# Kernel tuning notes

Measured on AMD Instinct MI355X. Metric: run time of the kernel, lower is better.

Reference implementation:

```python
import jax, jax.numpy as jnp
import numpy as np

C_M, C_Z, C_H = 256, 128, 32
S, N = 128, 384
EPS = 1e-5


def setup_inputs() -> dict:
    key = jax.random.key(0)
    ks = jax.random.split(key, 8)
    sc = 1.0 / np.sqrt(C_M)
    return {
        "msa": jax.random.normal(ks[0], (S, N, C_M), dtype=jnp.float32),
        "ln_g": jnp.ones((C_M,), dtype=jnp.float32),
        "ln_b": jnp.zeros((C_M,), dtype=jnp.float32),
        "Wl": jax.random.uniform(ks[1], (C_M, C_H), jnp.float32, -sc, sc),
        "bl": jax.random.uniform(ks[2], (C_H,), jnp.float32, -sc, sc),
        "Wr": jax.random.uniform(ks[3], (C_M, C_H), jnp.float32, -sc, sc),
        "br": jax.random.uniform(ks[4], (C_H,), jnp.float32, -sc, sc),
        "Wo": jax.random.uniform(ks[5], (C_H * C_H, C_Z), jnp.float32, -1.0 / C_H, 1.0 / C_H),
        "bo": jax.random.uniform(ks[6], (C_Z,), jnp.float32, -1.0 / C_H, 1.0 / C_H),
    }


def _layernorm(x, g, b):
    mu = jnp.mean(x, axis=-1, keepdims=True)
    var = jnp.mean(jnp.square(x - mu), axis=-1, keepdims=True)
    return (x - mu) * jax.lax.rsqrt(var + EPS) * g + b


def reference(msa, ln_g, ln_b, Wl, bl, Wr, br, Wo, bo):
    s = msa.shape[0]
    m = _layernorm(msa, ln_g, ln_b)          # [s, n, c_m]
    left = m @ Wl + bl                        # [s, n, c_h]
    right = m @ Wr + br                       # [s, n, c_h]
    outer = jnp.einsum('sic,sjd->ijcd', left, right) / s  # [n, n, c_h, c_h]
    outer = outer.reshape(outer.shape[0], outer.shape[1], -1)
    return outer @ Wo + bo                    # [n, n, c_z]
```

## Files before the change

kernel.cpp:

```cpp
#include <hip/hip_runtime.h>
#include <hip/hip_bf16.h>

#define CM 256
#define CZ 128
#define CH 32
#define SS 128
#define NN 384

typedef short bf16x8 __attribute__((ext_vector_type(8)));
typedef float f32x4 __attribute__((ext_vector_type(4)));
typedef unsigned short us4 __attribute__((ext_vector_type(4)));
typedef unsigned short us8 __attribute__((ext_vector_type(8)));

__device__ __forceinline__ unsigned short f2bf(float f) {
    __hip_bfloat16 h = __float2bfloat16(f);
    return __builtin_bit_cast(unsigned short, h);
}

__global__ __launch_bounds__(256) void k0_transpose(
    const float* __restrict__ Wo, const float* __restrict__ Wl, const float* __restrict__ Wr,
    unsigned short* __restrict__ WoT, unsigned short* __restrict__ WT) {
    int n = blockIdx.x;
    for (int k = threadIdx.x; k < CH * CH; k += blockDim.x) {
        WoT[n * (CH * CH) + k] = f2bf(Wo[(size_t)k * CZ + n]);
    }
    int k = threadIdx.x;
    if (n < 32) {
        WT[n * CM + k] = f2bf(Wl[(size_t)k * CH + n]);
    } else if (n < 64) {
        WT[32 * CM + (n - 32) * CM + k] = f2bf(Wr[(size_t)k * CH + (n - 32)]);
    }
}

__global__ __launch_bounds__(256, 2) void k1_ln_proj(
    const float* __restrict__ msa, const float* __restrict__ g, const float* __restrict__ bta,
    const unsigned short* __restrict__ WT, const float* __restrict__ bl, const float* __restrict__ br,
    unsigned short* __restrict__ Lt, unsigned short* __restrict__ Rt)
{
    __shared__ unsigned short A_lds[64 * 264];
    __shared__ unsigned short B_lds[64 * 264];

    const int i    = blockIdx.x;
    const int sh   = blockIdx.y;
    const int t    = threadIdx.x;
    const int wv   = t >> 6;
    const int lane = t & 63;
    const int lr   = lane & 15, lg = lane >> 4;

    const float4 gv = ((const float4*)g)[lane];
    const float4 bv = ((const float4*)bta)[lane];
#pragma unroll 4
    for (int r = 0; r < 16; r++) {
        int sl = wv * 16 + r;
        int s  = sh * 64 + sl;
        float4 v = ((const float4*)(msa + ((size_t)s * NN + i) * CM))[lane];
        float sum = v.x + v.y + v.z + v.w;
        float sq  = v.x * v.x + v.y * v.y + v.z * v.z + v.w * v.w;
#pragma unroll
        for (int off = 32; off >= 1; off >>= 1) {
            sum += __shfl_xor(sum, off, 64);
            sq  += __shfl_xor(sq, off, 64);
        }
        float mu = sum * (1.f / CM);
        float rs = rsqrtf(sq * (1.f / CM) - mu * mu + 1e-5f);
        us4 pk;
        pk[0] = f2bf((v.x - mu) * rs * gv.x + bv.x);
        pk[1] = f2bf((v.y - mu) * rs * gv.y + bv.y);
        pk[2] = f2bf((v.z - mu) * rs * gv.z + bv.z);
        pk[3] = f2bf((v.w - mu) * rs * gv.w + bv.w);
        *(us4*)&A_lds[sl * 264 + lane * 4] = pk;
    }
#pragma unroll
    for (int u = 0; u < 8; u++) {
        int id = u * 256 + t;
        *(us8*)&B_lds[(id >> 5) * 264 + (id & 31) * 8] = *(const us8*)&WT[id * 8];
    }
    __syncthreads();

    const int m0 = (wv >> 1) * 32;
    const int n0 = (wv & 1) * 32;
    f32x4 acc[2][2];
#pragma unroll
    for (int a = 0; a < 2; a++)
#pragma unroll
        for (int b = 0; b < 2; b++) acc[a][b] = (f32x4){0.f, 0.f, 0.f, 0.f};

#pragma unroll
    for (int ks = 0; ks < 8; ks++) {
        int ko = ks * 32 + lg * 8;
        bf16x8 a0 = *(const bf16x8*)&A_lds[(m0 + lr) * 264 + ko];
        bf16x8 a1 = *(const bf16x8*)&A_lds[(m0 + 16 + lr) * 264 + ko];
        bf16x8 b0 = *(const bf16x8*)&B_lds[(n0 + lr) * 264 + ko];
        bf16x8 b1 = *(const bf16x8*)&B_lds[(n0 + 16 + lr) * 264 + ko];
        acc[0][0] = __builtin_amdgcn_mfma_f32_16x16x32_bf16(a0, b0, acc[0][0], 0, 0, 0);
        acc[0][1] = __builtin_amdgcn_mfma_f32_16x16x32_bf16(a0, b1, acc[0][1], 0, 0, 0);
        acc[1][0] = __builtin_amdgcn_mfma_f32_16x16x32_bf16(a1, b0, acc[1][0], 0, 0, 0);
        acc[1][1] = __builtin_amdgcn_mfma_f32_16x16x32_bf16(a1, b1, acc[1][1], 0, 0, 0);
    }

    const bool isL = (n0 == 0);
    const float scale = isL ? 0.0078125f : 1.f;
#pragma unroll
    for (int mt = 0; mt < 2; mt++)
#pragma unroll
        for (int nt = 0; nt < 2; nt++) {
            int ch = (n0 + nt * 16 + lr) & 31;
            float bias = isL ? bl[ch] : br[ch];
            us4 pk;
#pragma unroll
            for (int rg = 0; rg < 4; rg++)
                pk[rg] = f2bf((acc[mt][nt][rg] + bias) * scale);
            unsigned short* dst = (isL ? Lt : Rt) + (size_t)(i * CH + ch) * SS
                                  + sh * 64 + m0 + mt * 16 + lg * 4;
            *(us4*)dst = pk;
        }
}

#define TI 8
#define TJ 8
#define P1_B_OFF 69632
#define OH1_OFF  65536
#define WO_OFF   131072
#define K2_LDS   163840

__global__ __launch_bounds__(512, 2) void k2_fused(
    const unsigned short* __restrict__ Lt, const unsigned short* __restrict__ Rt,
    const unsigned short* __restrict__ WoT, const float* __restrict__ bo,
    float* __restrict__ out)
{
    extern __shared__ char smem[];
    unsigned short* A = (unsigned short*)(smem);
    unsigned short* B = (unsigned short*)(smem + P1_B_OFF);

    const int i0 = blockIdx.x * TI;
    const int j0 = blockIdx.y * TJ;
    const int t  = threadIdx.x;
    const int wv = t >> 6, lane = t & 63;
    const int lr = lane & 15, lg = lane >> 4;

    const unsigned short* gA = Lt + (size_t)i0 * CH * SS;
    const unsigned short* gB = Rt + (size_t)j0 * CH * SS;
#pragma unroll
    for (int it = 0; it < 8; it++) {
        int c  = it * 512 + t;
        int rw = c >> 4, kc = c & 15;
        *(us8*)(A + rw * 136 + kc * 8) = *(const us8*)(gA + rw * 128 + kc * 8);
        *(us8*)(B + rw * 136 + kc * 8) = *(const us8*)(gB + rw * 128 + kc * 8);
    }
    __syncthreads();

    const int m0  = (wv >> 2) * 128;
    const int n0w = (wv & 3) * 64;

    f32x4 accE[4][4], accO[4][4];
#pragma unroll
    for (int a = 0; a < 4; a++)
#pragma unroll
        for (int b = 0; b < 4; b++) {
            accE[a][b] = (f32x4){0.f, 0.f, 0.f, 0.f};
            accO[a][b] = (f32x4){0.f, 0.f, 0.f, 0.f};
        }

#pragma unroll
    for (int ks = 0; ks < 4; ks++) {
        int ko = ks * 32 + lg * 8;
        bf16x8 af[8], bfr[4];
#pragma unroll
        for (int mt = 0; mt < 8; mt++) af[mt]  = *(const bf16x8*)(A + (m0 + mt * 16 + lr) * 136 + ko);
#pragma unroll
        for (int nt = 0; nt < 4; nt++) bfr[nt] = *(const bf16x8*)(B + (n0w + nt * 16 + lr) * 136 + ko);
#pragma unroll
        for (int mt = 0; mt < 8; mt++)
#pragma unroll
            for (int nt = 0; nt < 4; nt++) {
                if (mt & 1)
                    accO[mt >> 1][nt] = __builtin_amdgcn_mfma_f32_16x16x32_bf16(bfr[nt], af[mt], accO[mt >> 1][nt], 0, 0, 0);
                else
                    accE[mt >> 1][nt] = __builtin_amdgcn_mfma_f32_16x16x32_bf16(bfr[nt], af[mt], accE[mt >> 1][nt], 0, 0, 0);
            }
    }
    __syncthreads();

    us8 wreg[4];
#pragma unroll
    for (int q = 0; q < 4; q++) {
        int lam = q * 512 + t;
        int z = lam >> 4, cc = lam & 15;
        int cg = cc ^ (z & 15);
        wreg[q] = *(const us8*)&WoT[(size_t)z * 1024 + cg * 8];
    }

    {
        unsigned short* Oh0 = (unsigned short*)smem;
        unsigned short* Oh1 = (unsigned short*)(smem + OH1_OFF);
#pragma unroll
        for (int mh = 0; mh < 4; mh++) {
            int iiw  = (wv >> 2) * 4 + mh;
            int rowH = iiw * 16 + lr;
            int okey = (rowH ^ (rowH >> 4)) & 7;
#pragma unroll
            for (int nt = 0; nt < 4; nt++) {
                int colBase = n0w + nt * 16 + lg * 4;
                int chk = (colBase >> 3) ^ okey;
                int off = rowH * 256 + chk * 8 + (lg & 1) * 4;
                us4 pkE, pkO;
#pragma unroll
                for (int rg = 0; rg < 4; rg++) {
                    pkE[rg] = f2bf(accE[mh][nt][rg]);
                    pkO[rg] = f2bf(accO[mh][nt][rg]);
                }
                *(us4*)&Oh0[off] = pkE;
                *(us4*)&Oh1[off] = pkO;
            }
        }
    }

    const int zsl = wv & 1, ksl = wv >> 1;
    unsigned short* WB = (unsigned short*)(smem + WO_OFF);

    f32x4 acc2[4][4];
#pragma unroll
    for (int a = 0; a < 4; a++)
#pragma unroll
        for (int b = 0; b < 4; b++) acc2[a][b] = (f32x4){0.f, 0.f, 0.f, 0.f};

    for (int c = 0; c < 8; c++) {
        __syncthreads();
#pragma unroll
        for (int q = 0; q < 4; q++) {
            int lam = q * 512 + t;
            *(us8*)&WB[lam * 8] = wreg[q];
        }
        if (c < 7) {
#pragma unroll
            for (int q = 0; q < 4; q++) {
                int lam = q * 512 + t;
                int z = lam >> 4, cc = lam & 15;
                int cg = cc ^ (z & 15);
                wreg[q] = *(const us8*)&WoT[(size_t)z * 1024 + (c + 1) * 128 + cg * 8];
            }
        }
        __syncthreads();

        const int cch = c * 4 + ksl;
        const int hh  = cch >> 4;
        const int cH  = cch & 15;
        const unsigned short* OhX = (const unsigned short*)(smem + (hh ? OH1_OFF : 0));

        bf16x8 af2[4], bf2[4];
#pragma unroll
        for (int ai = 0; ai < 4; ai++) {
            int rowH = (ai * 2 + ((lane >> 3) & 1)) * 16 + cH;
            int okey = (rowH ^ (rowH >> 4)) & 7;
            int chk  = (((lane & 7) * 4 + lg) ^ okey);
            af2[ai] = *(const bf16x8*)&OhX[rowH * 256 + chk * 8];
        }
#pragma unroll
        for (int bi = 0; bi < 4; bi++) {
            int z = zsl * 64 + bi * 16 + lr;
            int chk = (ksl * 4 + lg) ^ (z & 15);
            bf2[bi] = *(const bf16x8*)&WB[z * 128 + chk * 8];
        }
#pragma unroll
        for (int ai = 0; ai < 4; ai++)
#pragma unroll
            for (int bi = 0; bi < 4; bi++)
                acc2[ai][bi] = __builtin_amdgcn_mfma_f32_16x16x32_bf16(af2[ai], bf2[bi], acc2[ai][bi], 0, 0, 0);
    }
    __syncthreads();

    float* RB = (float*)smem;
#pragma unroll
    for (int ai = 0; ai < 4; ai++)
#pragma unroll
        for (int bi = 0; bi < 4; bi++) {
            int z  = zsl * 64 + bi * 16 + lr;
            int pr = ai * 16 + lg * 4;
            *(f32x4*)&RB[ksl * 8704 + z * 68 + pr] = acc2[ai][bi];
        }
    __syncthreads();

    {
        int z = t >> 2, pq = t & 3;
        float bz = bo[z];
#pragma unroll
        for (int u = 0; u < 4; u++) {
            int p0r = pq * 16 + u * 4;
            f32x4 s = (f32x4){0.f, 0.f, 0.f, 0.f};
#pragma unroll
            for (int ks2 = 0; ks2 < 4; ks2++)
                s += *(const f32x4*)&RB[ks2 * 8704 + z * 68 + p0r];
#pragma unroll
            for (int e = 0; e < 4; e++) {
                int p = p0r + e;
                out[((size_t)(i0 + (p >> 3)) * NN + (j0 + (p & 7))) * CZ + z] = s[e] + bz;
            }
        }
    }
}

extern "C" void kernel_launch(void* const* d_in, const int* in_sizes, int n_in,
                              void* d_out, int out_size, void* d_ws, size_t ws_size,
                              hipStream_t stream) {
    const float* msa  = (const float*)d_in[0];
    const float* ln_g = (const float*)d_in[1];
    const float* ln_b = (const float*)d_in[2];
    const float* Wl   = (const float*)d_in[3];
    const float* bl   = (const float*)d_in[4];
    const float* Wr   = (const float*)d_in[5];
    const float* br   = (const float*)d_in[6];
    const float* Wo   = (const float*)d_in[7];
    const float* bo   = (const float*)d_in[8];
    float* out = (float*)d_out;

    unsigned short* Lt  = (unsigned short*)d_ws;
    unsigned short* Rt  = Lt + (size_t)NN * CH * SS;
    unsigned short* WoT = Rt + (size_t)NN * CH * SS;
    unsigned short* WT  = WoT + (size_t)CZ * CH * CH;

    hipFuncSetAttribute((const void*)k2_fused,
                        hipFuncAttributeMaxDynamicSharedMemorySize, K2_LDS);

    k0_transpose<<<dim3(CZ), dim3(256), 0, stream>>>(Wo, Wl, Wr, WoT, WT);
    k1_ln_proj<<<dim3(NN, 2), dim3(256), 0, stream>>>(msa, ln_g, ln_b, WT, bl, br, Lt, Rt);
    k2_fused<<<dim3(NN / TI, NN / TJ), dim3(512), K2_LDS, stream>>>(Lt, Rt, WoT, bo, out);
}
```

Measured before the change: 219.7 us.

## Pre-swizzle Wo into MFMA fragment order and load B operands directly from global

The Wo weight is rearranged once into per-lane MFMA fragment order, so each wave in the second GEMM loads its B operands straight from global/L2 into registers and double-buffers them. The LDS staging buffer for Wo and the two barriers per K-chunk go away, and LDS use drops from 160KB to 136KB. The cost is that each wave now issues its own global loads (duplicated across the row-tile waves and across blocks) and register pressure rises from holding two sets of fragments.

```diff
diff --git a/kernel.cpp b/kernel.cpp
--- a/kernel.cpp
+++ b/kernel.cpp
@@ -19,10 +19,17 @@
 
 __global__ __launch_bounds__(256) void k0_transpose(
     const float* __restrict__ Wo, const float* __restrict__ Wl, const float* __restrict__ Wr,
-    unsigned short* __restrict__ WoT, unsigned short* __restrict__ WT) {
+    unsigned short* __restrict__ WoF, unsigned short* __restrict__ WT) {
     int n = blockIdx.x;
-    for (int k = threadIdx.x; k < CH * CH; k += blockDim.x) {
-        WoT[n * (CH * CH) + k] = f2bf(Wo[(size_t)k * CZ + n]);
+    int base = n * 1024;
+#pragma unroll
+    for (int u = 0; u < 4; u++) {
+        int w   = base + u * 256 + threadIdx.x;
+        int e   = w & 7;
+        int l   = (w >> 3) & 63;
+        int zb  = (w >> 9) & 7;
+        int cch = w >> 12;
+        WoF[w] = f2bf(Wo[(size_t)(cch * 32 + (l >> 4) * 8 + e) * CZ + zb * 16 + (l & 15)]);
     }
     int k = threadIdx.x;
     if (n < 32) {
@@ -120,12 +127,11 @@
 #define TJ 8
 #define P1_B_OFF 69632
 #define OH1_OFF  65536
-#define WO_OFF   131072
-#define K2_LDS   163840
+#define K2_LDS   139264
 
 __global__ __launch_bounds__(512, 2) void k2_fused(
     const unsigned short* __restrict__ Lt, const unsigned short* __restrict__ Rt,
-    const unsigned short* __restrict__ WoT, const float* __restrict__ bo,
+    const unsigned short* __restrict__ WoF, const float* __restrict__ bo,
     float* __restrict__ out)
 {
     extern __shared__ char smem[];
@@ -181,14 +187,12 @@
     }
     __syncthreads();
 
-    us8 wreg[4];
-#pragma unroll
-    for (int q = 0; q < 4; q++) {
-        int lam = q * 512 + t;
-        int z = lam >> 4, cc = lam & 15;
-        int cg = cc ^ (z & 15);
-        wreg[q] = *(const us8*)&WoT[(size_t)z * 1024 + cg * 8];
-    }
+    const int zsl = wv & 1, ksl = wv >> 1;
+
+    bf16x8 wcur[4], wnxt[4];
+#pragma unroll
+    for (int bi = 0; bi < 4; bi++)
+        wcur[bi] = *(const bf16x8*)&WoF[(((size_t)ksl * 8 + zsl * 4 + bi) * 64 + lane) * 8];
 
     {
         unsigned short* Oh0 = (unsigned short*)smem;
@@ -214,9 +218,7 @@
             }
         }
     }
-
-    const int zsl = wv & 1, ksl = wv >> 1;
-    unsigned short* WB = (unsigned short*)(smem + WO_OFF);
+    __syncthreads();
 
     f32x4 acc2[4][4];
 #pragma unroll
@@ -224,30 +226,21 @@
 #pragma unroll
         for (int b = 0; b < 4; b++) acc2[a][b] = (f32x4){0.f, 0.f, 0.f, 0.f};
 
+#pragma unroll
     for (int c = 0; c < 8; c++) {
-        __syncthreads();
-#pragma unroll
-        for (int q = 0; q < 4; q++) {
-            int lam = q * 512 + t;
-            *(us8*)&WB[lam * 8] = wreg[q];
-        }
         if (c < 7) {
-#pragma unroll
-            for (int q = 0; q < 4; q++) {
-                int lam = q * 512 + t;
-                int z = lam >> 4, cc = lam & 15;
-                int cg = cc ^ (z & 15);
-                wreg[q] = *(const us8*)&WoT[(size_t)z * 1024 + (c + 1) * 128 + cg * 8];
-            }
-        }
-        __syncthreads();
+            int cchn = (c + 1) * 4 + ksl;
+#pragma unroll
+            for (int bi = 0; bi < 4; bi++)
+                wnxt[bi] = *(const bf16x8*)&WoF[(((size_t)cchn * 8 + zsl * 4 + bi) * 64 + lane) * 8];
+        }
 
         const int cch = c * 4 + ksl;
         const int hh  = cch >> 4;
         const int cH  = cch & 15;
         const unsigned short* OhX = (const unsigned short*)(smem + (hh ? OH1_OFF : 0));
 
-        bf16x8 af2[4], bf2[4];
+        bf16x8 af2[4];
 #pragma unroll
         for (int ai = 0; ai < 4; ai++) {
             int rowH = (ai * 2 + ((lane >> 3) & 1)) * 16 + cH;
@@ -256,16 +249,15 @@
             af2[ai] = *(const bf16x8*)&OhX[rowH * 256 + chk * 8];
         }
 #pragma unroll
-        for (int bi = 0; bi < 4; bi++) {
-            int z = zsl * 64 + bi * 16 + lr;
-            int chk = (ksl * 4 + lg) ^ (z & 15);
-            bf2[bi] = *(const bf16x8*)&WB[z * 128 + chk * 8];
-        }
-#pragma unroll
         for (int ai = 0; ai < 4; ai++)
 #pragma unroll
             for (int bi = 0; bi < 4; bi++)
-                acc2[ai][bi] = __builtin_amdgcn_mfma_f32_16x16x32_bf16(af2[ai], bf2[bi], acc2[ai][bi], 0, 0, 0);
+                acc2[ai][bi] = __builtin_amdgcn_mfma_f32_16x16x32_bf16(af2[ai], wcur[bi], acc2[ai][bi], 0, 0, 0);
+
+        if (c < 7) {
+#pragma unroll
+            for (int bi = 0; bi < 4; bi++) wcur[bi] = wnxt[bi];
+        }
     }
     __syncthreads();
 
@@ -315,13 +307,13 @@
 
     unsigned short* Lt  = (unsigned short*)d_ws;
     unsigned short* Rt  = Lt + (size_t)NN * CH * SS;
-    unsigned short* WoT = Rt + (size_t)NN * CH * SS;
-    unsigned short* WT  = WoT + (size_t)CZ * CH * CH;
+    unsigned short* WoF = Rt + (size_t)NN * CH * SS;
+    unsigned short* WT  = WoF + (size_t)CZ * CH * CH;
 
     hipFuncSetAttribute((const void*)k2_fused,
                         hipFuncAttributeMaxDynamicSharedMemorySize, K2_LDS);
 
-    k0_transpose<<<dim3(CZ), dim3(256), 0, stream>>>(Wo, Wl, Wr, WoT, WT);
+    k0_transpose<<<dim3(CZ), dim3(256), 0, stream>>>(Wo, Wl, Wr, WoF, WT);
     k1_ln_proj<<<dim3(NN, 2), dim3(256), 0, stream>>>(msa, ln_g, ln_b, WT, bl, br, Lt, Rt);
-    k2_fused<<<dim3(NN / TI, NN / TJ), dim3(512), K2_LDS, stream>>>(Lt, Rt, WoT, bo, out);
-}
+    k2_fused<<<dim3(NN / TI, NN / TJ), dim3(512), K2_LDS, stream>>>(Lt, Rt, WoF, bo, out);
+}
```

After: 206.7 us. -5.9%, faster.
